# Performance work log

Measured on AMD Instinct MI355X. Metric: run time of the kernel, lower is better.

The kernel has to match this reference:

```python
import jax, jax.numpy as jnp
import numpy as np

N = 40000        # total gene nodes
E = 640000       # edges
F_IN = 128       # num_features
H = 128          # hidden_dim
SUB = 400        # genes per cell
EPS = 1e-5


def _bn(x, g, b):
    # BatchNorm1d, training-mode batch statistics (biased variance), deterministic
    m = x.mean(axis=0)
    v = x.var(axis=0)
    return (x - m) * jax.lax.rsqrt(v + EPS) * g + b


def _gcn_conv(x, W, b, src, dst):
    # PyG GCNConv: h = X W; add self-loops; symmetric deg^{-1/2} normalization;
    # scatter-add messages from src into dst; then add bias.
    h = x @ W                                   # [N, H]
    loop = jnp.arange(N)
    s = jnp.concatenate([src, loop])            # [E+N]
    d = jnp.concatenate([dst, loop])
    deg = jax.ops.segment_sum(jnp.ones(s.shape[0], h.dtype), d, num_segments=N)
    dis = jnp.where(deg > 0, deg ** -0.5, 0.0)  # deg_inv_sqrt
    norm = dis[s] * dis[d]                      # [E+N]
    out = jax.ops.segment_sum(h[s] * norm[:, None], d, num_segments=N)
    return out + b


def setup_inputs() -> dict:
    key = jax.random.key(0)
    ks = jax.random.split(key, 16)
    sc = lambda fan: 1.0 / np.sqrt(fan)
    inp = {
        "x": jax.random.normal(ks[0], (N, F_IN), jnp.float32),
        "edge_index": jax.random.randint(ks[1], (2, E), 0, N, jnp.int64),
        "conv1_w": jax.random.normal(ks[2], (F_IN, H), jnp.float32) * sc(F_IN),
        "conv1_b": jnp.zeros((H,), jnp.float32),
        "bn1_g": jnp.ones((H,), jnp.float32),
        "bn1_b": jnp.zeros((H,), jnp.float32),
        "conv2_w": jax.random.normal(ks[3], (H, H), jnp.float32) * sc(H),
        "conv2_b": jnp.zeros((H,), jnp.float32),
        "bn2_g": jnp.ones((H,), jnp.float32),
        "bn2_b": jnp.zeros((H,), jnp.float32),
        "att_w1": jax.random.normal(ks[4], (H, H // 2), jnp.float32) * sc(H),
        "att_b1": jnp.zeros((H // 2,), jnp.float32),
        "att_w2": jax.random.normal(ks[5], (H // 2, 1), jnp.float32) * sc(H // 2),
        "att_b2": jnp.zeros((1,), jnp.float32),
        "fc_w": jax.random.normal(ks[6], (H, H), jnp.float32) * sc(H),
        "fc_b": jnp.zeros((H,), jnp.float32),
        "bne_g": jnp.ones((H,), jnp.float32),
        "bne_b": jnp.zeros((H,), jnp.float32),
        "bot_w": jax.random.normal(ks[7], (H, 32), jnp.float32) * sc(H),
        "bot_b": jnp.zeros((32,), jnp.float32),
        "bnb_g": jnp.ones((32,), jnp.float32),
        "bnb_b": jnp.zeros((32,), jnp.float32),
    }
    return inp


def reference(x, edge_index, conv1_w, conv1_b, bn1_g, bn1_b,
              conv2_w, conv2_b, bn2_g, bn2_b,
              att_w1, att_b1, att_w2, att_b2,
              fc_w, fc_b, bne_g, bne_b,
              bot_w, bot_b, bnb_g, bnb_b):
    src, dst = edge_index[0], edge_index[1]
    # embed: two GCNConv + BN + ReLU (dropout omitted: deterministic reference)
    h = jax.nn.relu(_bn(_gcn_conv(x, conv1_w, conv1_b, src, dst), bn1_g, bn1_b))
    emb = jax.nn.relu(_bn(_gcn_conv(h, conv2_w, conv2_b, src, dst), bn2_g, bn2_b))
    # attention pooling over genes within each cell
    num_cells = N // SUB
    xr = emb.reshape(num_cells, SUB, H)                      # [C, S, H]
    scores = jnp.tanh(xr @ att_w1 + att_b1) @ att_w2 + att_b2  # [C, S, 1]
    w = jax.nn.softmax(scores, axis=1)
    pooled = jnp.sum(xr * w, axis=1)                          # [C, H]
    # dense head
    y = jax.nn.relu(_bn(pooled @ fc_w + fc_b, bne_g, bne_b))
    y = jax.nn.relu(_bn(y @ bot_w + bot_b, bnb_g, bnb_b))     # [C, 32]
    return (y, emb)
```

## Files before the change

### kernel.cpp

```cpp
#include <hip/hip_runtime.h>
#include <math.h>

typedef unsigned int u32;
typedef unsigned short u16;
typedef __attribute__((ext_vector_type(8))) short bf16x8;
typedef __attribute__((ext_vector_type(4))) float f32x4;

#define NN   40000
#define EE   640000
#define SUBG 400
#define CELLS 100
#define BNEPS 1e-5f
#define GB    2048
#define GEMMB 625
#define DEGB  1024
#define FILLB 512

__device__ __forceinline__ u32 bf16pair(float a, float b) {
    u32 ua = __float_as_uint(a), ub = __float_as_uint(b);
    ua += 0x7fffu + ((ua >> 16) & 1u);
    ub += 0x7fffu + ((ub >> 16) & 1u);
    return (ua >> 16) | (ub & 0xffff0000u);
}
__device__ __forceinline__ float bflo(u32 u) { return __uint_as_float(u << 16); }
__device__ __forceinline__ float bfhi(u32 u) { return __uint_as_float(u & 0xffff0000u); }

__global__ __launch_bounds__(256)
void k_degW(const int* __restrict__ dst, int* __restrict__ deg,
            const float* __restrict__ W1, u32* __restrict__ Wt1,
            const float* __restrict__ W2, u32* __restrict__ Wt2,
            const float* __restrict__ wa, u32* __restrict__ Wta) {
    int bid = blockIdx.x;
    int t = threadIdx.x;
    if (bid < DEGB) {
        int i = bid * 256 + t;
        int stride = DEGB * 256;
        for (; i < EE; i += stride) atomicAdd(&deg[dst[i]], 1);
        return;
    }
    int i = (bid - DEGB) * 256 + t;
    if (i < 16384) {
        const float* W = (i < 8192) ? W1 : W2;
        u32* Wt = (i < 8192) ? Wt1 : Wt2;
        int j = i & 8191;
        int n = j >> 6, k2 = (j & 63) * 2;
        Wt[n * 64 + (j & 63)] = bf16pair(W[k2 * 128 + n], W[(k2 + 1) * 128 + n]);
        return;
    }
    i -= 16384;
    if (i < 4096) {
        int n = i >> 6, k2 = (i & 63) * 2;
        Wta[n * 64 + (i & 63)] = bf16pair(wa[k2 * 64 + n], wa[(k2 + 1) * 64 + n]);
    }
}

__global__ __launch_bounds__(1024)
void k_scan(const int* __restrict__ deg, int* __restrict__ rowstart,
            float* __restrict__ dis, float* __restrict__ hstats) {
    __shared__ int ps[1024];
    int t = threadIdx.x;
    if (t < 320) hstats[t] = 0.f;
    const int4* d4 = (const int4*)deg;
    int sum = 0;
#pragma unroll
    for (int j = 0; j < 10; ++j) {
        int i4 = t * 10 + j;
        if (i4 < 10000) {
            int4 v = d4[i4];
            sum += v.x + v.y + v.z + v.w;
        }
    }
    ps[t] = sum;
    __syncthreads();
    for (int off = 1; off < 1024; off <<= 1) {
        int add = (t >= off) ? ps[t - off] : 0;
        __syncthreads();
        ps[t] += add;
        __syncthreads();
    }
    int run = ps[t] - sum;
#pragma unroll
    for (int j = 0; j < 10; ++j) {
        int i4 = t * 10 + j;
        if (i4 < 10000) {
            int4 v = d4[i4];
            int4 r;
            r.x = run;
            r.y = run + v.x;
            r.z = r.y + v.y;
            r.w = r.z + v.z;
            run = r.w + v.w;
            *(int4*)&rowstart[i4 * 4] = r;
            float4 dv;
            dv.x = rsqrtf((float)(v.x + 1));
            dv.y = rsqrtf((float)(v.y + 1));
            dv.z = rsqrtf((float)(v.z + 1));
            dv.w = rsqrtf((float)(v.w + 1));
            *(float4*)&dis[i4 * 4] = dv;
        }
    }
    if (t == 0) rowstart[NN] = EE;
}

__global__ __launch_bounds__(256)
void k_fillgemm(const int* __restrict__ src, const int* __restrict__ dst,
                const int* __restrict__ rowstart, int* __restrict__ cursor,
                u16* __restrict__ csr16,
                const float* __restrict__ X, const u32* __restrict__ Wt,
                u32* __restrict__ Yb, const float* __restrict__ dis) {
    int bid = blockIdx.x;
    int t = threadIdx.x;
    if (bid < FILLB) {
        int g = bid & 7;
        int lo = g * (NN / 8), hi = lo + (NN / 8);
        int i = (bid >> 3) * 256 + t;
        int stride = (FILLB / 8) * 256;
        for (; i < EE; i += stride) {
            int d = dst[i];
            if (d >= lo && d < hi) {
                int slot = rowstart[d] + atomicAdd(&cursor[d], 1);
                csr16[slot] = (u16)src[i];
            }
        }
        return;
    }
    int l = t & 63, wv = t >> 6;
    int rowbase = (bid - FILLB) * 64 + wv * 16;
    int ml = l & 15, kg = l >> 4;

    f32x4 acc[8];
#pragma unroll
    for (int nt = 0; nt < 8; ++nt) acc[nt] = (f32x4){0.f, 0.f, 0.f, 0.f};
    const float* xr = X + (long)(rowbase + ml) * 128;
#pragma unroll
    for (int kk = 0; kk < 4; ++kk) {
        int k0 = kk * 32 + kg * 8;
        float4 xa = *(const float4*)&xr[k0];
        float4 xb = *(const float4*)&xr[k0 + 4];
        union { u32 u[4]; bf16x8 v; } af;
        af.u[0] = bf16pair(xa.x, xa.y);
        af.u[1] = bf16pair(xa.z, xa.w);
        af.u[2] = bf16pair(xb.x, xb.y);
        af.u[3] = bf16pair(xb.z, xb.w);
#pragma unroll
        for (int nt = 0; nt < 8; ++nt) {
            bf16x8 b = *(const bf16x8*)&Wt[(nt * 16 + ml) * 64 + (k0 >> 1)];
            acc[nt] = __builtin_amdgcn_mfma_f32_16x16x32_bf16(af.v, b, acc[nt], 0, 0, 0);
        }
    }
#pragma unroll
    for (int r = 0; r < 4; ++r) {
        int m = rowbase + kg * 4 + r;
        float dd = dis[m];
        long obase = (long)m * 64;
#pragma unroll
        for (int nt = 0; nt < 8; ++nt) {
            float v = acc[nt][r] * dd;
            float v2 = __shfl_xor(v, 1);
            if ((l & 1) == 0)
                Yb[obase + nt * 8 + (ml >> 1)] = bf16pair(v, v2);
        }
    }
}

__global__ __launch_bounds__(256)
void k_gemm_bf16(const u32* __restrict__ Xb, const u32* __restrict__ Wt,
                 u32* __restrict__ Yb, const float* __restrict__ ss,
                 const float* __restrict__ dis) {
    int t = threadIdx.x;
    int l = t & 63, wv = t >> 6;
    int rowbase = blockIdx.x * 64 + wv * 16;
    int ml = l & 15, kg = l >> 4;

    f32x4 acc[8];
#pragma unroll
    for (int nt = 0; nt < 8; ++nt) acc[nt] = (f32x4){0.f, 0.f, 0.f, 0.f};
    const u32* xr = Xb + (long)(rowbase + ml) * 64;
#pragma unroll
    for (int kk = 0; kk < 4; ++kk) {
        int k0 = kk * 32 + kg * 8;
        uint4 xw = *(const uint4*)&xr[k0 >> 1];
        float f0 = bflo(xw.x), f1 = bfhi(xw.x), f2 = bflo(xw.y), f3 = bfhi(xw.y);
        float f4 = bflo(xw.z), f5 = bfhi(xw.z), f6 = bflo(xw.w), f7 = bfhi(xw.w);
        float4 sca = *(const float4*)&ss[k0];
        float4 sha = *(const float4*)&ss[128 + k0];
        float4 scb = *(const float4*)&ss[k0 + 4];
        float4 shb = *(const float4*)&ss[128 + k0 + 4];
        f0 = fmaxf(fmaf(f0, sca.x, sha.x), 0.f);
        f1 = fmaxf(fmaf(f1, sca.y, sha.y), 0.f);
        f2 = fmaxf(fmaf(f2, sca.z, sha.z), 0.f);
        f3 = fmaxf(fmaf(f3, sca.w, sha.w), 0.f);
        f4 = fmaxf(fmaf(f4, scb.x, shb.x), 0.f);
        f5 = fmaxf(fmaf(f5, scb.y, shb.y), 0.f);
        f6 = fmaxf(fmaf(f6, scb.z, shb.z), 0.f);
        f7 = fmaxf(fmaf(f7, scb.w, shb.w), 0.f);
        union { u32 u[4]; bf16x8 v; } af;
        af.u[0] = bf16pair(f0, f1);
        af.u[1] = bf16pair(f2, f3);
        af.u[2] = bf16pair(f4, f5);
        af.u[3] = bf16pair(f6, f7);
#pragma unroll
        for (int nt = 0; nt < 8; ++nt) {
            bf16x8 b = *(const bf16x8*)&Wt[(nt * 16 + ml) * 64 + (k0 >> 1)];
            acc[nt] = __builtin_amdgcn_mfma_f32_16x16x32_bf16(af.v, b, acc[nt], 0, 0, 0);
        }
    }
#pragma unroll
    for (int r = 0; r < 4; ++r) {
        int m = rowbase + kg * 4 + r;
        float dd = dis[m];
        long obase = (long)m * 64;
#pragma unroll
        for (int nt = 0; nt < 8; ++nt) {
            float v = acc[nt][r] * dd;
            float v2 = __shfl_xor(v, 1);
            if ((l & 1) == 0)
                Yb[obase + nt * 8 + (ml >> 1)] = bf16pair(v, v2);
        }
    }
}

__global__ __launch_bounds__(256)
void k_gather_stats(const uint4* __restrict__ Hb, const int* __restrict__ rowstart,
                    const u16* __restrict__ csr16, const float* __restrict__ dis,
                    const float* __restrict__ bias, u32* __restrict__ F1b,
                    float* __restrict__ part) {
    __shared__ float ls[1024], lq[1024];
    int t = threadIdx.x;
    int lane = t & 63, wv = t >> 6;
    int gw = blockIdx.x * 4 + wv;
    int g = lane >> 4, p = lane & 15;
    int c0 = p * 8 + g * 2;
    float2 bb = *(const float2*)&bias[c0];
    float s0 = 0.f, s1 = 0.f, q0 = 0.f, q1 = 0.f;

    for (int node = gw; node < NN; node += GB * 4) {
        float a0 = 0.f, a1 = 0.f, a2 = 0.f, a3 = 0.f, a4 = 0.f, a5 = 0.f, a6 = 0.f, a7 = 0.f;
        if (g == 0) {
            uint4 h = Hb[node * 16 + p];
            a0 = bflo(h.x); a1 = bfhi(h.x);
            a2 = bflo(h.y); a3 = bfhi(h.y);
            a4 = bflo(h.z); a5 = bfhi(h.z);
            a6 = bflo(h.w); a7 = bfhi(h.w);
        }
        int e1 = rowstart[node + 1];
        int e = rowstart[node] + g;
        for (; e + 4 < e1; e += 8) {
            int sA = csr16[e];
            int sB = csr16[e + 4];
            uint4 h0 = Hb[sA * 16 + p];
            uint4 h1 = Hb[sB * 16 + p];
            a0 += bflo(h0.x); a1 += bfhi(h0.x);
            a2 += bflo(h0.y); a3 += bfhi(h0.y);
            a4 += bflo(h0.z); a5 += bfhi(h0.z);
            a6 += bflo(h0.w); a7 += bfhi(h0.w);
            a0 += bflo(h1.x); a1 += bfhi(h1.x);
            a2 += bflo(h1.y); a3 += bfhi(h1.y);
            a4 += bflo(h1.z); a5 += bfhi(h1.z);
            a6 += bflo(h1.w); a7 += bfhi(h1.w);
        }
        if (e < e1) {
            int sA = csr16[e];
            uint4 h0 = Hb[sA * 16 + p];
            a0 += bflo(h0.x); a1 += bfhi(h0.x);
            a2 += bflo(h0.y); a3 += bfhi(h0.y);
            a4 += bflo(h0.z); a5 += bfhi(h0.z);
            a6 += bflo(h0.w); a7 += bfhi(h0.w);
        }
#pragma unroll
        for (int m = 16; m <= 32; m <<= 1) {
            a0 += __shfl_xor(a0, m); a1 += __shfl_xor(a1, m);
            a2 += __shfl_xor(a2, m); a3 += __shfl_xor(a3, m);
            a4 += __shfl_xor(a4, m); a5 += __shfl_xor(a5, m);
            a6 += __shfl_xor(a6, m); a7 += __shfl_xor(a7, m);
        }
        float dd = dis[node];
        float x = (g == 0) ? a0 : (g == 1) ? a2 : (g == 2) ? a4 : a6;
        float y = (g == 0) ? a1 : (g == 1) ? a3 : (g == 2) ? a5 : a7;
        x = fmaf(x, dd, bb.x);
        y = fmaf(y, dd, bb.y);
        u32 pw = bf16pair(x, y);
        F1b[node * 64 + (c0 >> 1)] = pw;
        float rx = bflo(pw), ry = bfhi(pw);
        s0 += rx; s1 += ry; q0 += rx * rx; q1 += ry * ry;
    }
    ls[wv * 128 + c0] = s0; ls[wv * 128 + c0 + 1] = s1;
    lq[wv * 128 + c0] = q0; lq[wv * 128 + c0 + 1] = q1;
    __syncthreads();
    if (t < 128) {
        float S = ls[t] + ls[128 + t] + ls[256 + t] + ls[384 + t];
        float Q = lq[t] + lq[128 + t] + lq[256 + t] + lq[384 + t];
        part[blockIdx.x * 256 + t] = S;
        part[blockIdx.x * 256 + 128 + t] = Q;
    }
}

__global__ __launch_bounds__(256)
void k_bnfinalw(const float* __restrict__ part, const float* __restrict__ g,
                const float* __restrict__ b, float* __restrict__ ss) {
    __shared__ float rs[256], rq[256];
    int c = blockIdx.x, t = threadIdx.x;
    float s = 0.f, q = 0.f;
    for (int i = t; i < GB; i += 256) {
        s += part[i * 256 + c];
        q += part[i * 256 + 128 + c];
    }
    rs[t] = s; rq[t] = q;
    __syncthreads();
    for (int off = 128; off > 0; off >>= 1) {
        if (t < off) { rs[t] += rs[t + off]; rq[t] += rq[t + off]; }
        __syncthreads();
    }
    if (t == 0) {
        float mean = rs[0] * (1.0f / NN);
        float var  = rq[0] * (1.0f / NN) - mean * mean;
        float sc = g[c] * rsqrtf(var + BNEPS);
        ss[c] = sc;
        ss[128 + c] = b[c] - mean * sc;
    }
}

__global__ __launch_bounds__(256)
void k_scoremb(const u32* __restrict__ F1b, const float* __restrict__ ss,
               float* __restrict__ emb,
               const u32* __restrict__ Wta, const float* __restrict__ b1,
               const float* __restrict__ w2, const float* __restrict__ b2,
               float* __restrict__ scores) {
    int t = threadIdx.x;
    int l = t & 63, wv = t >> 6;
    int rowbase = blockIdx.x * 64 + wv * 16;
    int ml = l & 15, kg = l >> 4;

    f32x4 acc[4];
#pragma unroll
    for (int nt = 0; nt < 4; ++nt) acc[nt] = (f32x4){0.f, 0.f, 0.f, 0.f};
    const u32* xr = F1b + (long)(rowbase + ml) * 64;
    float* er = emb + (long)(rowbase + ml) * 128;
#pragma unroll
    for (int kk = 0; kk < 4; ++kk) {
        int k0 = kk * 32 + kg * 8;
        uint4 xw = *(const uint4*)&xr[k0 >> 1];
        float f0 = bflo(xw.x), f1 = bfhi(xw.x), f2 = bflo(xw.y), f3 = bfhi(xw.y);
        float f4 = bflo(xw.z), f5 = bfhi(xw.z), f6 = bflo(xw.w), f7 = bfhi(xw.w);
        float4 sca = *(const float4*)&ss[k0];
        float4 sha = *(const float4*)&ss[128 + k0];
        float4 scb = *(const float4*)&ss[k0 + 4];
        float4 shb = *(const float4*)&ss[128 + k0 + 4];
        f0 = fmaxf(fmaf(f0, sca.x, sha.x), 0.f);
        f1 = fmaxf(fmaf(f1, sca.y, sha.y), 0.f);
        f2 = fmaxf(fmaf(f2, sca.z, sha.z), 0.f);
        f3 = fmaxf(fmaf(f3, sca.w, sha.w), 0.f);
        f4 = fmaxf(fmaf(f4, scb.x, shb.x), 0.f);
        f5 = fmaxf(fmaf(f5, scb.y, shb.y), 0.f);
        f6 = fmaxf(fmaf(f6, scb.z, shb.z), 0.f);
        f7 = fmaxf(fmaf(f7, scb.w, shb.w), 0.f);
        float4 e0 = { f0, f1, f2, f3 };
        float4 e1 = { f4, f5, f6, f7 };
        *(float4*)&er[k0] = e0;
        *(float4*)&er[k0 + 4] = e1;
        union { u32 u[4]; bf16x8 v; } af;
        af.u[0] = bf16pair(f0, f1);
        af.u[1] = bf16pair(f2, f3);
        af.u[2] = bf16pair(f4, f5);
        af.u[3] = bf16pair(f6, f7);
#pragma unroll
        for (int nt = 0; nt < 4; ++nt) {
            bf16x8 b = *(const bf16x8*)&Wta[(nt * 16 + ml) * 64 + (k0 >> 1)];
            acc[nt] = __builtin_amdgcn_mfma_f32_16x16x32_bf16(af.v, b, acc[nt], 0, 0, 0);
        }
    }
    float b1v[4], w2v[4];
#pragma unroll
    for (int nt = 0; nt < 4; ++nt) {
        b1v[nt] = b1[nt * 16 + ml];
        w2v[nt] = w2[nt * 16 + ml];
    }
    float b2v = b2[0];
#pragma unroll
    for (int r = 0; r < 4; ++r) {
        float s = tanhf(acc[0][r] + b1v[0]) * w2v[0]
                + tanhf(acc[1][r] + b1v[1]) * w2v[1]
                + tanhf(acc[2][r] + b1v[2]) * w2v[2]
                + tanhf(acc[3][r] + b1v[3]) * w2v[3];
        s += __shfl_xor(s, 1);
        s += __shfl_xor(s, 2);
        s += __shfl_xor(s, 4);
        s += __shfl_xor(s, 8);
        if (ml == 0) scores[rowbase + kg * 4 + r] = s + b2v;
    }
}

__global__ __launch_bounds__(256)
void k_pool4(const u32* __restrict__ F1b, const float* __restrict__ ss,
             const float* __restrict__ scores, float* __restrict__ pp) {
    __shared__ float sl[SUBG];
    __shared__ float red[256];
    __shared__ float rbuf[512];
    int b = blockIdx.x;
    int c = b >> 2, q = b & 3;
    int t = threadIdx.x;
    int base = c * SUBG;

    float lmax = -1e30f;
    for (int i = t; i < SUBG; i += 256) {
        float v = scores[base + i];
        sl[i] = v;
        lmax = fmaxf(lmax, v);
    }
    red[t] = lmax;
    __syncthreads();
    for (int off = 128; off > 0; off >>= 1) {
        if (t < off) red[t] = fmaxf(red[t], red[t + off]);
        __syncthreads();
    }
    float mx = red[0];
    __syncthreads();
    float lsum = 0.f;
    for (int i = t; i < SUBG; i += 256) {
        float e = __expf(sl[i] - mx);
        sl[i] = e;
        lsum += e;
    }
    red[t] = lsum;
    __syncthreads();
    for (int off = 128; off > 0; off >>= 1) {
        if (t < off) red[t] += red[t + off];
        __syncthreads();
    }
    float inv = 1.0f / red[0];
    __syncthreads();

    int cc = t & 63, gp = t >> 6;
    float2 scv = *(const float2*)&ss[2 * cc];
    float2 shv = *(const float2*)&ss[128 + 2 * cc];
    int g0 = q * 100 + gp * 25;
    float a0 = 0.f, a1 = 0.f;
#pragma unroll 5
    for (int j = 0; j < 25; ++j) {
        int gg = g0 + j;
        u32 v = F1b[(long)(base + gg) * 64 + cc];
        float w = sl[gg] * inv;
        float x0 = fmaxf(fmaf(bflo(v), scv.x, shv.x), 0.f);
        float x1 = fmaxf(fmaf(bfhi(v), scv.y, shv.y), 0.f);
        a0 += w * x0;
        a1 += w * x1;
    }
    rbuf[gp * 128 + 2 * cc] = a0;
    rbuf[gp * 128 + 2 * cc + 1] = a1;
    __syncthreads();
    if (t < 128)
        pp[b * 128 + t] = rbuf[t] + rbuf[128 + t] + rbuf[256 + t] + rbuf[384 + t];
}

__global__ __launch_bounds__(128)
void k_head1r(const float* __restrict__ pp, const float* __restrict__ fc_w,
              const float* __restrict__ fc_b, float* __restrict__ y1pre,
              float* __restrict__ hstats) {
    __shared__ float pr[128];
    int c = blockIdx.x, t = threadIdx.x;
    pr[t] = pp[(c * 4 + 0) * 128 + t] + pp[(c * 4 + 1) * 128 + t]
          + pp[(c * 4 + 2) * 128 + t] + pp[(c * 4 + 3) * 128 + t];
    __syncthreads();
    float a1 = fc_b[t];
#pragma unroll 4
    for (int k = 0; k < 128; ++k) a1 = fmaf(pr[k], fc_w[k * 128 + t], a1);
    y1pre[c * 128 + t] = a1;
    atomicAdd(&hstats[t], a1);
    atomicAdd(&hstats[128 + t], a1 * a1);
}

__global__ __launch_bounds__(128)
void k_head2s(const float* __restrict__ y1pre, const float* __restrict__ hstats,
              const float* __restrict__ bne_g, const float* __restrict__ bne_b,
              const float* __restrict__ bot_w, const float* __restrict__ bot_b,
              float* __restrict__ y2pre, float* __restrict__ hstats2) {
    __shared__ float row[128];
    int c = blockIdx.x, t = threadIdx.x;
    float s = hstats[t], q = hstats[128 + t];
    float mean = s * 0.01f, var = q * 0.01f - mean * mean;
    float scv = bne_g[t] * rsqrtf(var + BNEPS);
    float shv = bne_b[t] - mean * scv;
    row[t] = fmaxf(fmaf(y1pre[c * 128 + t], scv, shv), 0.f);
    __syncthreads();
    if (t < 32) {
        float a2 = bot_b[t];
#pragma unroll 4
        for (int k = 0; k < 128; ++k) a2 = fmaf(row[k], bot_w[k * 32 + t], a2);
        y2pre[c * 32 + t] = a2;
        atomicAdd(&hstats2[t], a2);
        atomicAdd(&hstats2[32 + t], a2 * a2);
    }
}

__global__ __launch_bounds__(256)
void k_out(const float* __restrict__ y2pre, const float* __restrict__ hstats2,
           const float* __restrict__ bnb_g, const float* __restrict__ bnb_b,
           float* __restrict__ y_out) {
    __shared__ float scv[32], shv[32];
    int t = threadIdx.x;
    if (t < 32) {
        float s = hstats2[t], q = hstats2[32 + t];
        float mean = s * 0.01f, var = q * 0.01f - mean * mean;
        float v = bnb_g[t] * rsqrtf(var + BNEPS);
        scv[t] = v; shv[t] = bnb_b[t] - mean * v;
    }
    __syncthreads();
    for (int i = t; i < CELLS * 32; i += 256)
        y_out[i] = fmaxf(fmaf(y2pre[i], scv[i & 31], shv[i & 31]), 0.f);
}

extern "C" void kernel_launch(void* const* d_in, const int* in_sizes, int n_in,
                              void* d_out, int out_size, void* d_ws, size_t ws_size,
                              hipStream_t stream) {
    const float* x        = (const float*)d_in[0];
    const int*   ei       = (const int*)d_in[1];
    const float* conv1_w  = (const float*)d_in[2];
    const float* conv1_b  = (const float*)d_in[3];
    const float* bn1_g    = (const float*)d_in[4];
    const float* bn1_b    = (const float*)d_in[5];
    const float* conv2_w  = (const float*)d_in[6];
    const float* conv2_b  = (const float*)d_in[7];
    const float* bn2_g    = (const float*)d_in[8];
    const float* bn2_b    = (const float*)d_in[9];
    const float* att_w1   = (const float*)d_in[10];
    const float* att_b1   = (const float*)d_in[11];
    const float* att_w2   = (const float*)d_in[12];
    const float* att_b2   = (const float*)d_in[13];
    const float* fc_w     = (const float*)d_in[14];
    const float* fc_b     = (const float*)d_in[15];
    const float* bne_g    = (const float*)d_in[16];
    const float* bne_b    = (const float*)d_in[17];
    const float* bot_w    = (const float*)d_in[18];
    const float* bot_b    = (const float*)d_in[19];
    const float* bnb_g    = (const float*)d_in[20];
    const float* bnb_b    = (const float*)d_in[21];

    const int* src = ei;
    const int* dst = ei + EE;

    float* y_out   = (float*)d_out;
    float* emb_out = y_out + CELLS * 32;

    float* ws = (float*)d_ws;
    u32*   Hb     = (u32*)ws;
    u32*   F1b    = Hb + (long)NN * 64;
    float* dis    = (float*)(F1b + (long)NN * 64);
    float* part   = dis + NN;
    float* ss     = part + GB * 256;
    float* hstats = ss + 256;
    float* y1pre  = hstats + 320;
    float* y2pre  = y1pre + CELLS * 128;
    float* scores = y2pre + CELLS * 32;
    float* pp     = scores + NN;
    u32*   Wt1    = (u32*)(pp + 400 * 128);
    u32*   Wt2    = Wt1 + 8192;
    u32*   Wta    = Wt2 + 8192;
    int*   deg    = (int*)(Wta + 4096);
    int*   cursor = deg + NN;
    int*   rowstart = cursor + NN;
    u16*   csr16  = (u16*)(rowstart + NN + 1);

    hipMemsetAsync(deg, 0, (size_t)2 * NN * sizeof(int), stream);
    k_degW<<<DEGB + 80, 256, 0, stream>>>(dst, deg, conv1_w, Wt1, conv2_w, Wt2,
                                          att_w1, Wta);
    k_scan<<<1, 1024, 0, stream>>>(deg, rowstart, dis, hstats);
    k_fillgemm<<<FILLB + GEMMB, 256, 0, stream>>>(src, dst, rowstart, cursor, csr16,
                                                  x, Wt1, Hb, dis);
    k_gather_stats<<<GB, 256, 0, stream>>>((const uint4*)Hb, rowstart, csr16, dis,
                                           conv1_b, F1b, part);
    k_bnfinalw<<<128, 256, 0, stream>>>(part, bn1_g, bn1_b, ss);
    k_gemm_bf16<<<GEMMB, 256, 0, stream>>>(F1b, Wt2, Hb, ss, dis);
    k_gather_stats<<<GB, 256, 0, stream>>>((const uint4*)Hb, rowstart, csr16, dis,
                                           conv2_b, F1b, part);
    k_bnfinalw<<<128, 256, 0, stream>>>(part, bn2_g, bn2_b, ss);
    k_scoremb<<<GEMMB, 256, 0, stream>>>(F1b, ss, emb_out, Wta, att_b1, att_w2,
                                         att_b2, scores);
    k_pool4<<<4 * CELLS, 256, 0, stream>>>(F1b, ss, scores, pp);
    k_head1r<<<CELLS, 128, 0, stream>>>(pp, fc_w, fc_b, y1pre, hstats);
    k_head2s<<<CELLS, 128, 0, stream>>>(y1pre, hstats, bne_g, bne_b, bot_w, bot_b,
                                        y2pre, hstats + 256);
    k_out<<<1, 256, 0, stream>>>(y2pre, hstats + 256, bnb_g, bnb_b, y_out);
}
```

Baseline: 242.7 us.

## Fold BN finalize into consumers, fuse head tail, simplify CSR fill

BatchNorm partial sums are now reduced with atomics into 8 slotted rows, and each consumer kernel (second GEMM, score, pool) computes the scale and shift itself. This removes two k_bnfinalw launches and the large partial buffer. The head2 and output kernels are merged into one single-block tail kernel, and the hstats zeroing moves into the memset. The CSR fill drops its 8-way destination partitioning in favour of a flat grid-stride loop with twice as many blocks. The cost is atomic contention on the stats rows, redundant BN finalize work in every block, and a single-block tail.

```diff
diff --git a/kernel.cpp b/kernel.cpp
--- a/kernel.cpp
+++ b/kernel.cpp
@@ -14,7 +14,7 @@
 #define GB    2048
 #define GEMMB 625
 #define DEGB  1024
-#define FILLB 512
+#define FILLB 1024
 
 __device__ __forceinline__ u32 bf16pair(float a, float b) {
     u32 ua = __float_as_uint(a), ub = __float_as_uint(b);
@@ -24,6 +24,26 @@
 }
 __device__ __forceinline__ float bflo(u32 u) { return __uint_as_float(u << 16); }
 __device__ __forceinline__ float bfhi(u32 u) { return __uint_as_float(u & 0xffff0000u); }
+
+__device__ __forceinline__ void bn_ss_from_part2(const float* __restrict__ part2,
+                                                 const float* __restrict__ bng,
+                                                 const float* __restrict__ bnb,
+                                                 float* ssc, float* ssh, int t) {
+    if (t < 128) {
+        float s = 0.f, q = 0.f;
+#pragma unroll
+        for (int g = 0; g < 8; ++g) {
+            s += part2[g * 256 + t];
+            q += part2[g * 256 + 128 + t];
+        }
+        float mean = s * (1.0f / NN);
+        float var  = q * (1.0f / NN) - mean * mean;
+        float sc = bng[t] * rsqrtf(var + BNEPS);
+        ssc[t] = sc;
+        ssh[t] = bnb[t] - mean * sc;
+    }
+    __syncthreads();
+}
 
 __global__ __launch_bounds__(256)
 void k_degW(const int* __restrict__ dst, int* __restrict__ deg,
@@ -56,10 +76,9 @@
 
 __global__ __launch_bounds__(1024)
 void k_scan(const int* __restrict__ deg, int* __restrict__ rowstart,
-            float* __restrict__ dis, float* __restrict__ hstats) {
+            float* __restrict__ dis) {
     __shared__ int ps[1024];
     int t = threadIdx.x;
-    if (t < 320) hstats[t] = 0.f;
     const int4* d4 = (const int4*)deg;
     int sum = 0;
 #pragma unroll
@@ -111,16 +130,12 @@
     int bid = blockIdx.x;
     int t = threadIdx.x;
     if (bid < FILLB) {
-        int g = bid & 7;
-        int lo = g * (NN / 8), hi = lo + (NN / 8);
-        int i = (bid >> 3) * 256 + t;
-        int stride = (FILLB / 8) * 256;
+        int i = bid * 256 + t;
+        int stride = FILLB * 256;
         for (; i < EE; i += stride) {
             int d = dst[i];
-            if (d >= lo && d < hi) {
-                int slot = rowstart[d] + atomicAdd(&cursor[d], 1);
-                csr16[slot] = (u16)src[i];
-            }
+            int slot = rowstart[d] + atomicAdd(&cursor[d], 1);
+            csr16[slot] = (u16)src[i];
         }
         return;
     }
@@ -164,67 +179,10 @@
 }
 
 __global__ __launch_bounds__(256)
-void k_gemm_bf16(const u32* __restrict__ Xb, const u32* __restrict__ Wt,
-                 u32* __restrict__ Yb, const float* __restrict__ ss,
-                 const float* __restrict__ dis) {
-    int t = threadIdx.x;
-    int l = t & 63, wv = t >> 6;
-    int rowbase = blockIdx.x * 64 + wv * 16;
-    int ml = l & 15, kg = l >> 4;
-
-    f32x4 acc[8];
-#pragma unroll
-    for (int nt = 0; nt < 8; ++nt) acc[nt] = (f32x4){0.f, 0.f, 0.f, 0.f};
-    const u32* xr = Xb + (long)(rowbase + ml) * 64;
-#pragma unroll
-    for (int kk = 0; kk < 4; ++kk) {
-        int k0 = kk * 32 + kg * 8;
-        uint4 xw = *(const uint4*)&xr[k0 >> 1];
-        float f0 = bflo(xw.x), f1 = bfhi(xw.x), f2 = bflo(xw.y), f3 = bfhi(xw.y);
-        float f4 = bflo(xw.z), f5 = bfhi(xw.z), f6 = bflo(xw.w), f7 = bfhi(xw.w);
-        float4 sca = *(const float4*)&ss[k0];
-        float4 sha = *(const float4*)&ss[128 + k0];
-        float4 scb = *(const float4*)&ss[k0 + 4];
-        float4 shb = *(const float4*)&ss[128 + k0 + 4];
-        f0 = fmaxf(fmaf(f0, sca.x, sha.x), 0.f);
-        f1 = fmaxf(fmaf(f1, sca.y, sha.y), 0.f);
-        f2 = fmaxf(fmaf(f2, sca.z, sha.z), 0.f);
-        f3 = fmaxf(fmaf(f3, sca.w, sha.w), 0.f);
-        f4 = fmaxf(fmaf(f4, scb.x, shb.x), 0.f);
-        f5 = fmaxf(fmaf(f5, scb.y, shb.y), 0.f);
-        f6 = fmaxf(fmaf(f6, scb.z, shb.z), 0.f);
-        f7 = fmaxf(fmaf(f7, scb.w, shb.w), 0.f);
-        union { u32 u[4]; bf16x8 v; } af;
-        af.u[0] = bf16pair(f0, f1);
-        af.u[1] = bf16pair(f2, f3);
-        af.u[2] = bf16pair(f4, f5);
-        af.u[3] = bf16pair(f6, f7);
-#pragma unroll
-        for (int nt = 0; nt < 8; ++nt) {
-            bf16x8 b = *(const bf16x8*)&Wt[(nt * 16 + ml) * 64 + (k0 >> 1)];
-            acc[nt] = __builtin_amdgcn_mfma_f32_16x16x32_bf16(af.v, b, acc[nt], 0, 0, 0);
-        }
-    }
-#pragma unroll
-    for (int r = 0; r < 4; ++r) {
-        int m = rowbase + kg * 4 + r;
-        float dd = dis[m];
-        long obase = (long)m * 64;
-#pragma unroll
-        for (int nt = 0; nt < 8; ++nt) {
-            float v = acc[nt][r] * dd;
-            float v2 = __shfl_xor(v, 1);
-            if ((l & 1) == 0)
-                Yb[obase + nt * 8 + (ml >> 1)] = bf16pair(v, v2);
-        }
-    }
-}
-
-__global__ __launch_bounds__(256)
 void k_gather_stats(const uint4* __restrict__ Hb, const int* __restrict__ rowstart,
                     const u16* __restrict__ csr16, const float* __restrict__ dis,
                     const float* __restrict__ bias, u32* __restrict__ F1b,
-                    float* __restrict__ part) {
+                    float* __restrict__ part2) {
     __shared__ float ls[1024], lq[1024];
     int t = threadIdx.x;
     int lane = t & 63, wv = t >> 6;
@@ -290,62 +248,103 @@
     if (t < 128) {
         float S = ls[t] + ls[128 + t] + ls[256 + t] + ls[384 + t];
         float Q = lq[t] + lq[128 + t] + lq[256 + t] + lq[384 + t];
-        part[blockIdx.x * 256 + t] = S;
-        part[blockIdx.x * 256 + 128 + t] = Q;
-    }
-}
-
-__global__ __launch_bounds__(256)
-void k_bnfinalw(const float* __restrict__ part, const float* __restrict__ g,
-                const float* __restrict__ b, float* __restrict__ ss) {
-    __shared__ float rs[256], rq[256];
-    int c = blockIdx.x, t = threadIdx.x;
-    float s = 0.f, q = 0.f;
-    for (int i = t; i < GB; i += 256) {
-        s += part[i * 256 + c];
-        q += part[i * 256 + 128 + c];
-    }
-    rs[t] = s; rq[t] = q;
-    __syncthreads();
-    for (int off = 128; off > 0; off >>= 1) {
-        if (t < off) { rs[t] += rs[t + off]; rq[t] += rq[t + off]; }
-        __syncthreads();
-    }
-    if (t == 0) {
-        float mean = rs[0] * (1.0f / NN);
-        float var  = rq[0] * (1.0f / NN) - mean * mean;
-        float sc = g[c] * rsqrtf(var + BNEPS);
-        ss[c] = sc;
-        ss[128 + c] = b[c] - mean * sc;
-    }
-}
-
-__global__ __launch_bounds__(256)
-void k_scoremb(const u32* __restrict__ F1b, const float* __restrict__ ss,
-               float* __restrict__ emb,
-               const u32* __restrict__ Wta, const float* __restrict__ b1,
-               const float* __restrict__ w2, const float* __restrict__ b2,
-               float* __restrict__ scores) {
-    int t = threadIdx.x;
+        float* row = part2 + (blockIdx.x & 7) * 256;
+        atomicAdd(&row[t], S);
+        atomicAdd(&row[128 + t], Q);
+    }
+}
+
+__global__ __launch_bounds__(256)
+void k_gemm_bf16(const u32* __restrict__ Xb, const u32* __restrict__ Wt,
+                 u32* __restrict__ Yb, const float* __restrict__ part2,
+                 const float* __restrict__ bng, const float* __restrict__ bnb,
+                 const float* __restrict__ dis) {
+    __shared__ float ssc[128], ssh[128];
+    int t = threadIdx.x;
+    bn_ss_from_part2(part2, bng, bnb, ssc, ssh, t);
+
     int l = t & 63, wv = t >> 6;
     int rowbase = blockIdx.x * 64 + wv * 16;
     int ml = l & 15, kg = l >> 4;
 
-    f32x4 acc[4];
-#pragma unroll
-    for (int nt = 0; nt < 4; ++nt) acc[nt] = (f32x4){0.f, 0.f, 0.f, 0.f};
-    const u32* xr = F1b + (long)(rowbase + ml) * 64;
-    float* er = emb + (long)(rowbase + ml) * 128;
+    f32x4 acc[8];
+#pragma unroll
+    for (int nt = 0; nt < 8; ++nt) acc[nt] = (f32x4){0.f, 0.f, 0.f, 0.f};
+    const u32* xr = Xb + (long)(rowbase + ml) * 64;
 #pragma unroll
     for (int kk = 0; kk < 4; ++kk) {
         int k0 = kk * 32 + kg * 8;
         uint4 xw = *(const uint4*)&xr[k0 >> 1];
         float f0 = bflo(xw.x), f1 = bfhi(xw.x), f2 = bflo(xw.y), f3 = bfhi(xw.y);
         float f4 = bflo(xw.z), f5 = bfhi(xw.z), f6 = bflo(xw.w), f7 = bfhi(xw.w);
-        float4 sca = *(const float4*)&ss[k0];
-        float4 sha = *(const float4*)&ss[128 + k0];
-        float4 scb = *(const float4*)&ss[k0 + 4];
-        float4 shb = *(const float4*)&ss[128 + k0 + 4];
+        float4 sca = *(const float4*)&ssc[k0];
+        float4 sha = *(const float4*)&ssh[k0];
+        float4 scb = *(const float4*)&ssc[k0 + 4];
+        float4 shb = *(const float4*)&ssh[k0 + 4];
+        f0 = fmaxf(fmaf(f0, sca.x, sha.x), 0.f);
+        f1 = fmaxf(fmaf(f1, sca.y, sha.y), 0.f);
+        f2 = fmaxf(fmaf(f2, sca.z, sha.z), 0.f);
+        f3 = fmaxf(fmaf(f3, sca.w, sha.w), 0.f);
+        f4 = fmaxf(fmaf(f4, scb.x, shb.x), 0.f);
+        f5 = fmaxf(fmaf(f5, scb.y, shb.y), 0.f);
+        f6 = fmaxf(fmaf(f6, scb.z, shb.z), 0.f);
+        f7 = fmaxf(fmaf(f7, scb.w, shb.w), 0.f);
+        union { u32 u[4]; bf16x8 v; } af;
+        af.u[0] = bf16pair(f0, f1);
+        af.u[1] = bf16pair(f2, f3);
+        af.u[2] = bf16pair(f4, f5);
+        af.u[3] = bf16pair(f6, f7);
+#pragma unroll
+        for (int nt = 0; nt < 8; ++nt) {
+            bf16x8 b = *(const bf16x8*)&Wt[(nt * 16 + ml) * 64 + (k0 >> 1)];
+            acc[nt] = __builtin_amdgcn_mfma_f32_16x16x32_bf16(af.v, b, acc[nt], 0, 0, 0);
+        }
+    }
+#pragma unroll
+    for (int r = 0; r < 4; ++r) {
+        int m = rowbase + kg * 4 + r;
+        float dd = dis[m];
+        long obase = (long)m * 64;
+#pragma unroll
+        for (int nt = 0; nt < 8; ++nt) {
+            float v = acc[nt][r] * dd;
+            float v2 = __shfl_xor(v, 1);
+            if ((l & 1) == 0)
+                Yb[obase + nt * 8 + (ml >> 1)] = bf16pair(v, v2);
+        }
+    }
+}
+
+__global__ __launch_bounds__(256)
+void k_scoremb(const u32* __restrict__ F1b, const float* __restrict__ part2,
+               const float* __restrict__ bng, const float* __restrict__ bnb,
+               float* __restrict__ emb,
+               const u32* __restrict__ Wta, const float* __restrict__ b1,
+               const float* __restrict__ w2, const float* __restrict__ b2,
+               float* __restrict__ scores) {
+    __shared__ float ssc[128], ssh[128];
+    int t = threadIdx.x;
+    bn_ss_from_part2(part2, bng, bnb, ssc, ssh, t);
+
+    int l = t & 63, wv = t >> 6;
+    int rowbase = blockIdx.x * 64 + wv * 16;
+    int ml = l & 15, kg = l >> 4;
+
+    f32x4 acc[4];
+#pragma unroll
+    for (int nt = 0; nt < 4; ++nt) acc[nt] = (f32x4){0.f, 0.f, 0.f, 0.f};
+    const u32* xr = F1b + (long)(rowbase + ml) * 64;
+    float* er = emb + (long)(rowbase + ml) * 128;
+#pragma unroll
+    for (int kk = 0; kk < 4; ++kk) {
+        int k0 = kk * 32 + kg * 8;
+        uint4 xw = *(const uint4*)&xr[k0 >> 1];
+        float f0 = bflo(xw.x), f1 = bfhi(xw.x), f2 = bflo(xw.y), f3 = bfhi(xw.y);
+        float f4 = bflo(xw.z), f5 = bfhi(xw.z), f6 = bflo(xw.w), f7 = bfhi(xw.w);
+        float4 sca = *(const float4*)&ssc[k0];
+        float4 sha = *(const float4*)&ssh[k0];
+        float4 scb = *(const float4*)&ssc[k0 + 4];
+        float4 shb = *(const float4*)&ssh[k0 + 4];
         f0 = fmaxf(fmaf(f0, sca.x, sha.x), 0.f);
         f1 = fmaxf(fmaf(f1, sca.y, sha.y), 0.f);
         f2 = fmaxf(fmaf(f2, sca.z, sha.z), 0.f);
@@ -391,8 +390,10 @@
 }
 
 __global__ __launch_bounds__(256)
-void k_pool4(const u32* __restrict__ F1b, const float* __restrict__ ss,
+void k_pool4(const u32* __restrict__ F1b, const float* __restrict__ part2,
+             const float* __restrict__ bng, const float* __restrict__ bnb,
              const float* __restrict__ scores, float* __restrict__ pp) {
+    __shared__ float ssc[128], ssh[128];
     __shared__ float sl[SUBG];
     __shared__ float red[256];
     __shared__ float rbuf[512];
@@ -400,6 +401,7 @@
     int c = b >> 2, q = b & 3;
     int t = threadIdx.x;
     int base = c * SUBG;
+    bn_ss_from_part2(part2, bng, bnb, ssc, ssh, t);
 
     float lmax = -1e30f;
     for (int i = t; i < SUBG; i += 256) {
@@ -431,8 +433,8 @@
     __syncthreads();
 
     int cc = t & 63, gp = t >> 6;
-    float2 scv = *(const float2*)&ss[2 * cc];
-    float2 shv = *(const float2*)&ss[128 + 2 * cc];
+    float2 scv = *(const float2*)&ssc[2 * cc];
+    float2 shv = *(const float2*)&ssh[2 * cc];
     int g0 = q * 100 + gp * 25;
     float a0 = 0.f, a1 = 0.f;
 #pragma unroll 5
@@ -469,44 +471,55 @@
     atomicAdd(&hstats[128 + t], a1 * a1);
 }
 
-__global__ __launch_bounds__(128)
-void k_head2s(const float* __restrict__ y1pre, const float* __restrict__ hstats,
-              const float* __restrict__ bne_g, const float* __restrict__ bne_b,
-              const float* __restrict__ bot_w, const float* __restrict__ bot_b,
-              float* __restrict__ y2pre, float* __restrict__ hstats2) {
-    __shared__ float row[128];
-    int c = blockIdx.x, t = threadIdx.x;
-    float s = hstats[t], q = hstats[128 + t];
-    float mean = s * 0.01f, var = q * 0.01f - mean * mean;
-    float scv = bne_g[t] * rsqrtf(var + BNEPS);
-    float shv = bne_b[t] - mean * scv;
-    row[t] = fmaxf(fmaf(y1pre[c * 128 + t], scv, shv), 0.f);
+__global__ __launch_bounds__(256)
+void k_tail(const float* __restrict__ y1pre, const float* __restrict__ hstats,
+            const float* __restrict__ bne_g, const float* __restrict__ bne_b,
+            const float* __restrict__ bot_w, const float* __restrict__ bot_b,
+            const float* __restrict__ bnb_g, const float* __restrict__ bnb_b,
+            float* __restrict__ y_out) {
+    __shared__ float Y1[CELLS * 128];
+    __shared__ float Y2[CELLS * 32];
+    __shared__ float sc1[128], sh1[128];
+    __shared__ float red[256], red2[256];
+    int t = threadIdx.x;
+    if (t < 128) {
+        float s = hstats[t], q = hstats[128 + t];
+        float mean = s * 0.01f, var = q * 0.01f - mean * mean;
+        float sc = bne_g[t] * rsqrtf(var + BNEPS);
+        sc1[t] = sc; sh1[t] = bne_b[t] - mean * sc;
+    }
+    __syncthreads();
+    for (int i = t; i < CELLS * 128; i += 256) {
+        int col = i & 127;
+        Y1[i] = fmaxf(fmaf(y1pre[i], sc1[col], sh1[col]), 0.f);
+    }
+    __syncthreads();
+
+    int col2 = t & 31, g2 = t >> 5;
+    float s2 = 0.f, q2 = 0.f;
+    for (int j = 0; j < 13; ++j) {
+        int c = g2 + 8 * j;
+        if (c < CELLS) {
+            float a = bot_b[col2];
+#pragma unroll 4
+            for (int k = 0; k < 128; ++k) a = fmaf(Y1[c * 128 + k], bot_w[k * 32 + col2], a);
+            Y2[c * 32 + col2] = a;
+            s2 += a; q2 += a * a;
+        }
+    }
+    red[t] = s2; red2[t] = q2;
     __syncthreads();
     if (t < 32) {
-        float a2 = bot_b[t];
-#pragma unroll 4
-        for (int k = 0; k < 128; ++k) a2 = fmaf(row[k], bot_w[k * 32 + t], a2);
-        y2pre[c * 32 + t] = a2;
-        atomicAdd(&hstats2[t], a2);
-        atomicAdd(&hstats2[32 + t], a2 * a2);
-    }
-}
-
-__global__ __launch_bounds__(256)
-void k_out(const float* __restrict__ y2pre, const float* __restrict__ hstats2,
-           const float* __restrict__ bnb_g, const float* __restrict__ bnb_b,
-           float* __restrict__ y_out) {
-    __shared__ float scv[32], shv[32];
-    int t = threadIdx.x;
-    if (t < 32) {
-        float s = hstats2[t], q = hstats2[32 + t];
-        float mean = s * 0.01f, var = q * 0.01f - mean * mean;
+        float S = 0.f, Q = 0.f;
+#pragma unroll
+        for (int u = 0; u < 8; ++u) { S += red[u * 32 + t]; Q += red2[u * 32 + t]; }
+        float mean = S * 0.01f, var = Q * 0.01f - mean * mean;
         float v = bnb_g[t] * rsqrtf(var + BNEPS);
-        scv[t] = v; shv[t] = bnb_b[t] - mean * v;
+        red[t] = v; red2[t] = bnb_b[t] - mean * v;
     }
     __syncthreads();
     for (int i = t; i < CELLS * 32; i += 256)
-        y_out[i] = fmaxf(fmaf(y2pre[i], scv[i & 31], shv[i & 31]), 0.f);
+        y_out[i] = fmaxf(fmaf(Y2[i], red[i & 31], red2[i & 31]), 0.f);
 }
 
 extern "C" void kernel_launch(void* const* d_in, const int* in_sizes, int n_in,
@@ -545,39 +558,35 @@
     u32*   Hb     = (u32*)ws;
     u32*   F1b    = Hb + (long)NN * 64;
     float* dis    = (float*)(F1b + (long)NN * 64);
-    float* part   = dis + NN;
-    float* ss     = part + GB * 256;
-    float* hstats = ss + 256;
-    float* y1pre  = hstats + 320;
-    float* y2pre  = y1pre + CELLS * 128;
-    float* scores = y2pre + CELLS * 32;
+    float* y1pre  = dis + NN;
+    float* scores = y1pre + CELLS * 128;
     float* pp     = scores + NN;
     u32*   Wt1    = (u32*)(pp + 400 * 128);
     u32*   Wt2    = Wt1 + 8192;
     u32*   Wta    = Wt2 + 8192;
     int*   deg    = (int*)(Wta + 4096);
     int*   cursor = deg + NN;
-    int*   rowstart = cursor + NN;
+    float* part2A = (float*)(cursor + NN);
+    float* part2B = part2A + 2048;
+    float* hstats = part2B + 2048;
+    int*   rowstart = (int*)(hstats + 256);
     u16*   csr16  = (u16*)(rowstart + NN + 1);
 
-    hipMemsetAsync(deg, 0, (size_t)2 * NN * sizeof(int), stream);
+    hipMemsetAsync(deg, 0, (size_t)(2 * NN + 2048 + 2048 + 256) * sizeof(int), stream);
     k_degW<<<DEGB + 80, 256, 0, stream>>>(dst, deg, conv1_w, Wt1, conv2_w, Wt2,
                                           att_w1, Wta);
-    k_scan<<<1, 1024, 0, stream>>>(deg, rowstart, dis, hstats);
+    k_scan<<<1, 1024, 0, stream>>>(deg, rowstart, dis);
     k_fillgemm<<<FILLB + GEMMB, 256, 0, stream>>>(src, dst, rowstart, cursor, csr16,
                                                   x, Wt1, Hb, dis);
     k_gather_stats<<<GB, 256, 0, stream>>>((const uint4*)Hb, rowstart, csr16, dis,
-                                           conv1_b, F1b, part);
-    k_bnfinalw<<<128, 256, 0, stream>>>(part, bn1_g, bn1_b, ss);
-    k_gemm_bf16<<<GEMMB, 256, 0, stream>>>(F1b, Wt2, Hb, ss, dis);
+                                           conv1_b, F1b, part2A);
+    k_gemm_bf16<<<GEMMB, 256, 0, stream>>>(F1b, Wt2, Hb, part2A, bn1_g, bn1_b, dis);
     k_gather_stats<<<GB, 256, 0, stream>>>((const uint4*)Hb, rowstart, csr16, dis,
-                                           conv2_b, F1b, part);
-    k_bnfinalw<<<128, 256, 0, stream>>>(part, bn2_g, bn2_b, ss);
-    k_scoremb<<<GEMMB, 256, 0, stream>>>(F1b, ss, emb_out, Wta, att_b1, att_w2,
-                                         att_b2, scores);
-    k_pool4<<<4 * CELLS, 256, 0, stream>>>(F1b, ss, scores, pp);
+                                           conv2_b, F1b, part2B);
+    k_scoremb<<<GEMMB, 256, 0, stream>>>(F1b, part2B, bn2_g, bn2_b, emb_out,
+                                         Wta, att_b1, att_w2, att_b2, scores);
+    k_pool4<<<4 * CELLS, 256, 0, stream>>>(F1b, part2B, bn2_g, bn2_b, scores, pp);
     k_head1r<<<CELLS, 128, 0, stream>>>(pp, fc_w, fc_b, y1pre, hstats);
-    k_head2s<<<CELLS, 128, 0, stream>>>(y1pre, hstats, bne_g, bne_b, bot_w, bot_b,
-                                        y2pre, hstats + 256);
-    k_out<<<1, 256, 0, stream>>>(y2pre, hstats + 256, bnb_g, bnb_b, y_out);
-}
+    k_tail<<<1, 256, 0, stream>>>(y1pre, hstats, bne_g, bne_b, bot_w, bot_b,
+                                  bnb_g, bnb_b, y_out);
+}
```

Result: slower. 255.7 us (+5.3%).
